# Kernel tuning notes

Measured on AMD Instinct MI355X. Metric: run time of the kernel, lower is better.

The kernel has to match this reference:

```python
import jax, jax.numpy as jnp
import numpy as np

BINS = 128

def setup_inputs() -> dict:
    key = jax.random.key(0)
    k1, k2 = jax.random.split(key)
    B, S, F = 32, 16384, 64
    x = jax.random.uniform(k1, (B, S, F), dtype=jnp.float32)  # normalized to [0,1)
    weights = jnp.ones((BINS, F), dtype=jnp.float32)  # module inits weights to 1
    return {"input": x, "weights": weights}

def reference(input, weights):
    # input: [B, S, F]; weights: [bins, F]
    B, S, F = input.shape
    bins = weights.shape[0]
    # bin index per point per feature, truncation like torch .int()
    idx = jnp.clip((input * bins).astype(jnp.int32), 0, bins - 1)  # [B,S,F]
    # composite segment id: (b*F + f)*bins + bin  -> histogram without one-hot blowup
    b_idx = jnp.arange(B, dtype=jnp.int32)[:, None, None]
    f_idx = jnp.arange(F, dtype=jnp.int32)[None, None, :]
    seg = (b_idx * F + f_idx) * bins + idx  # [B,S,F]
    hist_flat = jax.ops.segment_sum(
        jnp.ones(seg.size, dtype=input.dtype),
        seg.reshape(-1),
        num_segments=B * F * bins,
    )
    hist = hist_flat.reshape(B, F, bins).transpose(0, 2, 1)  # [B, bins, F]
    return hist * weights[None, :, :]
```

## Files before the change

kernel.cpp:

```cpp
#include <hip/hip_runtime.h>

#define BINS 128
#define FEAT 64
#define SEG (BINS * FEAT)
#define B_DIM 32
#define S_DIM 16384
#define CHUNKS 16
#define THREADS 512
#define UNROLL 8


__global__ __launch_bounds__(THREADS, 2)
void hist_part(const float* __restrict__ x, unsigned* __restrict__ part) {
    __shared__ unsigned hist[SEG];
    for (int i = threadIdx.x; i < SEG; i += THREADS) hist[i] = 0u;
    __syncthreads();

    const int b    = blockIdx.y;
    const int lane = threadIdx.x & 63;
    const int wave = threadIdx.x >> 6;
    const int chunk = S_DIM / CHUNKS;
    const int rows_per_wave = chunk / (THREADS / 64);

    const float* xb = x + (size_t)b * S_DIM * FEAT;
    const int s0 = blockIdx.x * chunk + wave * rows_per_wave;

    for (int it = 0; it < rows_per_wave; it += UNROLL) {
        float v[UNROLL];
        #pragma unroll
        for (int u = 0; u < UNROLL; ++u)
            v[u] = __builtin_nontemporal_load(
                       &xb[(size_t)(s0 + it + u) * FEAT + lane]);
        #pragma unroll
        for (int u = 0; u < UNROLL; ++u) {
            int bin = (int)(v[u] * 128.0f);
            bin = bin < 0 ? 0 : (bin > 127 ? 127 : bin);
            atomicAdd(&hist[(bin << 6) + lane], 1u);
        }
    }
    __syncthreads();

    unsigned* p = part + ((size_t)(b * CHUNKS + blockIdx.x)) * SEG;
    for (int i = threadIdx.x; i < SEG; i += THREADS)
        p[i] = hist[i];
}

__global__ __launch_bounds__(256)
void reduce_fin(const unsigned* __restrict__ part, float* __restrict__ out,
                const float* __restrict__ w) {
    int t = blockIdx.x * blockDim.x + threadIdx.x;
    if (t >= B_DIM * (SEG / 4)) return;
    int b = t >> 11;
    int q = t & 2047;
    const uint4* base = (const uint4*)(part + (size_t)b * CHUNKS * SEG) + q;
    unsigned s0 = 0, s1 = 0, s2 = 0, s3 = 0;
    #pragma unroll
    for (int c = 0; c < CHUNKS; ++c) {
        uint4 v = base[(size_t)c * (SEG / 4)];
        s0 += v.x; s1 += v.y; s2 += v.z; s3 += v.w;
    }
    float4 wv = ((const float4*)w)[q];
    float4 o;
    o.x = (float)s0 * wv.x;
    o.y = (float)s1 * wv.y;
    o.z = (float)s2 * wv.z;
    o.w = (float)s3 * wv.w;
    ((float4*)out)[(size_t)b * (SEG / 4) + q] = o;
}


__global__ __launch_bounds__(THREADS, 2)
void hist_kernel(const float* __restrict__ x, unsigned* out) {
    __shared__ unsigned hist[SEG];
    for (int i = threadIdx.x; i < SEG; i += THREADS) hist[i] = 0u;
    __syncthreads();

    const int b    = blockIdx.y;
    const int lane = threadIdx.x & 63;
    const int wave = threadIdx.x >> 6;
    const int chunk = S_DIM / CHUNKS;
    const int rows_per_wave = chunk / (THREADS / 64);

    const float* xb = x + (size_t)b * S_DIM * FEAT;
    const int s0 = blockIdx.x * chunk + wave * rows_per_wave;

    for (int it = 0; it < rows_per_wave; it += UNROLL) {
        float v[UNROLL];
        #pragma unroll
        for (int u = 0; u < UNROLL; ++u)
            v[u] = xb[(size_t)(s0 + it + u) * FEAT + lane];
        #pragma unroll
        for (int u = 0; u < UNROLL; ++u) {
            int bin = (int)(v[u] * 128.0f);
            bin = bin < 0 ? 0 : (bin > 127 ? 127 : bin);
            atomicAdd(&hist[(bin << 6) + lane], 1u);
        }
    }
    __syncthreads();

    unsigned* gout = out + (size_t)b * SEG;
    for (int i = threadIdx.x; i < SEG; i += THREADS) {
        unsigned c = hist[i];
        if (c) atomicAdd(&gout[i], c);
    }
}

__global__ void finalize_kernel(const unsigned* cnt, float* out,
                                const float* __restrict__ w, int n) {
    int i = blockIdx.x * blockDim.x + threadIdx.x;
    if (i < n) {
        unsigned c = cnt[i];
        out[i] = (float)c * w[i & (SEG - 1)];
    }
}

extern "C" void kernel_launch(void* const* d_in, const int* in_sizes, int n_in,
                              void* d_out, int out_size, void* d_ws, size_t ws_size,
                              hipStream_t stream) {
    const float* x = (const float*)d_in[0];
    const float* w = (const float*)d_in[1];
    float* out = (float*)d_out;

    const size_t ws_needed = (size_t)B_DIM * CHUNKS * SEG * sizeof(unsigned);

    if (ws_size >= ws_needed && d_ws != nullptr) {
        unsigned* part = (unsigned*)d_ws;
        dim3 grid(CHUNKS, B_DIM);
        hist_part<<<grid, THREADS, 0, stream>>>(x, part);
        int nt = B_DIM * (SEG / 4);
        reduce_fin<<<(nt + 255) / 256, 256, 0, stream>>>(part, out, w);
    } else {
        hipMemsetAsync(d_out, 0, (size_t)out_size * sizeof(float), stream);
        dim3 grid(CHUNKS, B_DIM);
        hist_kernel<<<grid, THREADS, 0, stream>>>(x, (unsigned*)d_out);
        int n = out_size;
        finalize_kernel<<<(n + 255) / 256, 256, 0, stream>>>((const unsigned*)d_out, out, w, n);
    }
}
```

Measured before the change: 192.2 us.

## Fuse partial-histogram reduction into last block with 16-bit packed partials

```diff
diff --git a/kernel.cpp b/kernel.cpp
--- a/kernel.cpp
+++ b/kernel.cpp
@@ -8,12 +8,16 @@
 #define CHUNKS 16
 #define THREADS 512
 #define UNROLL 8
-
+#define PAIRS (SEG / 2)
 
 __global__ __launch_bounds__(THREADS, 2)
-void hist_part(const float* __restrict__ x, unsigned* __restrict__ part) {
+void hist_fused(const float* __restrict__ x, unsigned* __restrict__ part32,
+                unsigned* __restrict__ counters, float* __restrict__ out,
+                const float* __restrict__ w) {
     __shared__ unsigned hist[SEG];
-    for (int i = threadIdx.x; i < SEG; i += THREADS) hist[i] = 0u;
+    uint4* h4 = (uint4*)hist;
+    for (int i = threadIdx.x; i < SEG / 4; i += THREADS)
+        h4[i] = make_uint4(0u, 0u, 0u, 0u);
     __syncthreads();
 
     const int b    = blockIdx.y;
@@ -40,32 +44,50 @@
     }
     __syncthreads();
 
-    unsigned* p = part + ((size_t)(b * CHUNKS + blockIdx.x)) * SEG;
-    for (int i = threadIdx.x; i < SEG; i += THREADS)
-        p[i] = hist[i];
-}
+    unsigned* p = part32 + ((size_t)(b * CHUNKS + blockIdx.x)) * PAIRS;
+    for (int i = threadIdx.x; i < PAIRS; i += THREADS) {
+        unsigned lo = hist[2 * i], hi = hist[2 * i + 1];
+        p[i] = lo | (hi << 16);
+    }
 
-__global__ __launch_bounds__(256)
-void reduce_fin(const unsigned* __restrict__ part, float* __restrict__ out,
-                const float* __restrict__ w) {
-    int t = blockIdx.x * blockDim.x + threadIdx.x;
-    if (t >= B_DIM * (SEG / 4)) return;
-    int b = t >> 11;
-    int q = t & 2047;
-    const uint4* base = (const uint4*)(part + (size_t)b * CHUNKS * SEG) + q;
-    unsigned s0 = 0, s1 = 0, s2 = 0, s3 = 0;
+    __shared__ unsigned is_last;
+    __syncthreads();
+    if (threadIdx.x == 0) {
+        __threadfence();
+        unsigned old = atomicAdd(&counters[b], 1u);
+        is_last = (old == CHUNKS - 1) ? 1u : 0u;
+    }
+    __syncthreads();
+    if (!is_last) return;
+
+    __threadfence();
+
+    const unsigned* pb = part32 + (size_t)b * CHUNKS * PAIRS;
+    const int t = threadIdx.x;
+    unsigned slo[8] = {0, 0, 0, 0, 0, 0, 0, 0};
+    unsigned shi[8] = {0, 0, 0, 0, 0, 0, 0, 0};
+    for (int c = 0; c < CHUNKS; ++c) {
+        const uint4* q = (const uint4*)(pb + (size_t)c * PAIRS + t * 8);
+        uint4 a = q[0], d = q[1];
+        unsigned vv[8] = {a.x, a.y, a.z, a.w, d.x, d.y, d.z, d.w};
+        #pragma unroll
+        for (int j = 0; j < 8; ++j) {
+            slo[j] += vv[j] & 0xFFFFu;
+            shi[j] += vv[j] >> 16;
+        }
+    }
+    const float4* w4 = (const float4*)(w + t * 16);
+    float4* o4 = (float4*)(out + (size_t)b * SEG + t * 16);
     #pragma unroll
-    for (int c = 0; c < CHUNKS; ++c) {
-        uint4 v = base[(size_t)c * (SEG / 4)];
-        s0 += v.x; s1 += v.y; s2 += v.z; s3 += v.w;
+    for (int k = 0; k < 4; ++k) {
+        float4 wv = w4[k];
+        float4 o;
+        o.x = (float)slo[2 * k]     * wv.x;
+        o.y = (float)shi[2 * k]     * wv.y;
+        o.z = (float)slo[2 * k + 1] * wv.z;
+        o.w = (float)shi[2 * k + 1] * wv.w;
+        o4[k] = o;
     }
-    float4 wv = ((const float4*)w)[q];
-    float4 o;
-    o.x = (float)s0 * wv.x;
-    o.y = (float)s1 * wv.y;
-    o.z = (float)s2 * wv.z;
-    o.w = (float)s3 * wv.w;
-    ((float4*)out)[(size_t)b * (SEG / 4) + q] = o;
 }
 
 
@@ -121,14 +143,15 @@
     const float* w = (const float*)d_in[1];
     float* out = (float*)d_out;
 
-    const size_t ws_needed = (size_t)B_DIM * CHUNKS * SEG * sizeof(unsigned);
+    const size_t part_bytes = (size_t)B_DIM * CHUNKS * PAIRS * sizeof(unsigned);
+    const size_t ws_needed  = part_bytes + 128;
 
     if (ws_size >= ws_needed && d_ws != nullptr) {
-        unsigned* part = (unsigned*)d_ws;
+        unsigned* part32   = (unsigned*)d_ws;
+        unsigned* counters = (unsigned*)((char*)d_ws + part_bytes);
+        hipMemsetAsync(counters, 0, B_DIM * sizeof(unsigned), stream);
         dim3 grid(CHUNKS, B_DIM);
-        hist_part<<<grid, THREADS, 0, stream>>>(x, part);
-        int nt = B_DIM * (SEG / 4);
-        reduce_fin<<<(nt + 255) / 256, 256, 0, stream>>>(part, out, w);
+        hist_fused<<<grid, THREADS, 0, stream>>>(x, part32, counters, out, w);
     } else {
         hipMemsetAsync(d_out, 0, (size_t)out_size * sizeof(float), stream);
         dim3 grid(CHUNKS, B_DIM);
```

Measured after the change: 229.9 us. +19.6%, slower.
